# Kernel tuning notes

Measured on AMD Instinct MI355X. Metric: run time of the kernel, lower is better.

The kernel has to match this reference:

```python
import jax, jax.numpy as jnp
import numpy as np
from jax import lax

B, T, D, H, S = 256, 512, 256, 512, 8


def setup_inputs() -> dict:
    key = jax.random.key(0)
    ks = jax.random.split(key, 8)
    bound = 1.0 / np.sqrt(H)  # torch LSTMCell/Linear default init scale
    u = lambda k_, shp: jax.random.uniform(k_, shp, jnp.float32, -bound, bound)
    _input = jax.random.normal(ks[0], (B, T, D), jnp.float32)
    h0 = jax.random.normal(ks[1], (B, H), jnp.float32)
    c0 = jax.random.normal(ks[2], (B, H), jnp.float32)
    W_ih = u(ks[3], (4 * H, D))
    W_hh = u(ks[4], (4 * H, H))
    b_ih = u(ks[5], (4 * H,))
    b_hh = u(ks[6], (4 * H,))
    W_lin = u(ks[7], (D, H))
    b_lin = jnp.zeros((D,), jnp.float32)
    # random skip weights per module logic: w1~Bern; w2=1 if w1==0 else Bern; first S steps (1,0)
    rng = np.random.default_rng(0)
    w1 = rng.integers(0, 2, T)
    w2 = np.where(w1 == 0, 1, rng.integers(0, 2, T))
    w1[:S] = 1
    w2[:S] = 0
    return {
        "_input": _input, "h0": h0, "c0": c0,
        "W_ih": W_ih, "W_hh": W_hh, "b_ih": b_ih, "b_hh": b_hh,
        "W_lin": W_lin, "b_lin": b_lin,
        "w1": jnp.asarray(w1, jnp.int32), "w2": jnp.asarray(w2, jnp.int32),
        "time_steps": T, "skip_size": S,
    }


def _lstm_cell(x, h, c, W_ih, W_hh, b_ih, b_hh):
    gates = x @ W_ih.T + b_ih + h @ W_hh.T + b_hh  # [B, 4H]
    i, f, g, o = jnp.split(gates, 4, axis=-1)
    i, f, o = jax.nn.sigmoid(i), jax.nn.sigmoid(f), jax.nn.sigmoid(o)
    c_new = f * c + i * jnp.tanh(g)
    h_new = o * jnp.tanh(c_new)
    return h_new, c_new


def reference(_input, h0, c0, W_ih, W_hh, b_ih, b_hh, W_lin, b_lin, w1, w2, time_steps, skip_size):
    # decoder-mode RSCN: feed previous linear(h) as next input
    buf_h = jnp.repeat(h0[None], skip_size, axis=0)  # FIFO queue as ring buffer [S,B,H]
    buf_c = jnp.repeat(c0[None], skip_size, axis=0)

    def step(carry, xs):
        h_feed, h, c, bh, bc = carry
        w1t, w2t, t = xs
        h_new, c_new = _lstm_cell(h_feed, h, c, W_ih, W_hh, b_ih, b_hh)
        pos = t % skip_size
        skip_h, skip_c = bh[pos], bc[pos]  # queue.get() (oldest)
        bh = bh.at[pos].set(h_new)          # queue.put(new)
        bc = bc.at[pos].set(c_new)
        a = w1t.astype(h_new.dtype)
        b = w2t.astype(h_new.dtype)
        norm = 1.0 / (a + b)
        comb_h = (a * h_new + b * jnp.tanh(skip_h)) * norm
        comb_c = (a * c_new + b * jnp.tanh(skip_c)) * norm
        out = comb_h @ W_lin.T + b_lin  # [B, D]
        return (out, comb_h, comb_c, bh, bc), out

    xs = (w1[:time_steps], w2[:time_steps], jnp.arange(time_steps))
    carry0 = (_input[:, 0, :], h0, c0, buf_h, buf_c)
    (_, h_fin, c_fin, _, _), outs = lax.scan(step, carry0, xs)
    return outs.transpose(1, 0, 2), h_fin, c_fin  # [B,T,D], final (h, c)
```

## Files before the change

kernel.cpp:

```cpp
#include <hip/hip_runtime.h>
#include <math.h>

#define BB 256
#define TT 512
#define DD 256
#define HH 512
#define SS 8
#define G4H 2048
#define BH (BB*HH)
#define OUT_BASE ((size_t)BB*TT*DD)
#define NGRP 16
#define GR 16
#define XSLOT_U32 4096

typedef _Float16 f16;
typedef __attribute__((ext_vector_type(8))) _Float16 f16x8;
typedef __attribute__((ext_vector_type(4))) float    f32x4;

__device__ __forceinline__ float sigm(float x) { return 1.f / (1.f + __expf(-x)); }
__device__ __forceinline__ float ftanh(float x) {
  x = fminf(15.f, fmaxf(-15.f, x));
  float e = __expf(-2.f * x);
  return (1.f - e) / (1.f + e);
}


__global__ __launch_bounds__(256) void prep_wbig16(
    const float* __restrict__ W_ih, const float* __restrict__ W_hh,
    const float* __restrict__ W_lin, f16* __restrict__ Wbig16)
{
  __shared__ float As[64][20];
  __shared__ float Bs[16][68];
  const int n0 = blockIdx.x * 64;
  const int j0 = blockIdx.y * 64;
  const int tid = threadIdx.x;
  const int tn = tid >> 4, tj = tid & 15;
  float acc[4][4] = {};
  for (int k0 = 0; k0 < DD; k0 += 16) {
    { int r = tid >> 2, c = (tid & 3) * 4;
      *(float4*)&As[r][c] = *(const float4*)&W_ih[(size_t)(n0 + r) * DD + k0 + c]; }
    { int r = tid >> 4, c = (tid & 15) * 4;
      *(float4*)&Bs[r][c] = *(const float4*)&W_lin[(size_t)(k0 + r) * HH + j0 + c]; }
    __syncthreads();
    #pragma unroll
    for (int k = 0; k < 16; ++k) {
      float a[4], bv[4];
      #pragma unroll
      for (int i = 0; i < 4; ++i) a[i] = As[tn*4+i][k];
      #pragma unroll
      for (int m = 0; m < 4; ++m) bv[m] = Bs[k][tj*4+m];
      #pragma unroll
      for (int i = 0; i < 4; ++i)
        #pragma unroll
        for (int m = 0; m < 4; ++m)
          acc[i][m] = fmaf(a[i], bv[m], acc[i][m]);
    }
    __syncthreads();
  }
  #pragma unroll
  for (int i = 0; i < 4; ++i) {
    int n = n0 + tn*4 + i;
    #pragma unroll
    for (int m = 0; m < 4; ++m) {
      int j = j0 + tj*4 + m;
      Wbig16[(size_t)n*HH + j] = (f16)(acc[i][m] + W_hh[(size_t)n*HH + j]);
    }
  }
}

__global__ void prep_bias(const float* __restrict__ b_ih, const float* __restrict__ b_hh,
                          const float* __restrict__ W_ih, const float* __restrict__ b_lin,
                          float* __restrict__ bias0, float* __restrict__ bias1)
{
  int n = blockIdx.x * 256 + threadIdx.x;
  float s = b_ih[n] + b_hh[n];
  float d = 0.f;
  for (int k = 0; k < DD; ++k) d = fmaf(W_ih[(size_t)n*DD + k], b_lin[k], d);
  bias0[n] = s;
  bias1[n] = s + d;
}

#define NIH (G4H*DD)
#define NHH (G4H*HH)
__global__ void prep_cvtw(const float* __restrict__ W_ih, const float* __restrict__ W_hh,
                          const float* __restrict__ W_lin,
                          f16* __restrict__ Wih16, f16* __restrict__ Whh16,
                          f16* __restrict__ Wlin16)
{
  int e = blockIdx.x * 256 + threadIdx.x;
  if (e < NIH) Wih16[e] = (f16)W_ih[e];
  else if (e < NIH + NHH) Whh16[e - NIH] = (f16)W_hh[e - NIH];
  else Wlin16[e - NIH - NHH] = (f16)W_lin[e - NIH - NHH];
}

__global__ void prep_init(const float* __restrict__ x0, const float* __restrict__ h0,
                          const float* __restrict__ c0,
                          const int* __restrict__ w1, const int* __restrict__ w2,
                          float* __restrict__ bh, float* __restrict__ bc,
                          f16* __restrict__ x0hi, f16* __restrict__ x0lo,
                          f16* __restrict__ h0hi, f16* __restrict__ h0lo,
                          float4* __restrict__ stepc,
                          int* __restrict__ flags)
{
  int e = blockIdx.x * 256 + threadIdx.x;
  int r = e & (BH - 1);
  bh[e] = h0[r];
  bc[e] = c0[r];
  if (e < BH) {
    float v = h0[e];
    f16 hi = (f16)v;
    h0hi[e] = hi;
    h0lo[e] = (f16)(v - (float)hi);
  }
  if (e < BB*DD) {
    int b = e >> 8, d = e & 255;
    float v = x0[(size_t)b*(TT*DD) + d];
    f16 hi = (f16)v;
    x0hi[e] = hi;
    x0lo[e] = (f16)(v - (float)hi);
  }
  if (e < TT) {
    float a1 = (float)w1[e], a2 = (float)w2[e];
    stepc[e] = make_float4(a1, a2, 1.f / (a1 + a2), 0.f);
  }
  if (e < 256) flags[e] = 0;
}


__device__ __forceinline__ void stageG(const unsigned* __restrict__ Xs,
                                       f16* lds, int tid) {
  const int lane = tid & 63;
  const int wv = tid >> 6;
  #pragma unroll
  for (int i = 0; i < 2; ++i) {
    int r = wv * 2 + i;
    const char* src = (const char*)Xs + (size_t)r * 1024 +
                      (size_t)((lane ^ r) & 63) * 16;
    __builtin_amdgcn_global_load_lds(
        (const __attribute__((address_space(1))) void*)src,
        (__attribute__((address_space(3))) void*)((char*)lds + r * 1024),
        16, 0, 0x11 );
  }
}

__device__ __forceinline__ void gemm16(const f16x8 (&wA)[16], const f16x8 (&wB)[16],
                                       const f16* lds, int lane,
                                       f32x4& acc0, f32x4& acc1) {
  const int r  = lane & 15;
  const int kc = lane >> 4;
  const int rb = r * 1024;
  #pragma unroll
  for (int ks = 0; ks < 16; ++ks) {
    int u = ks * 4 + kc;
    f16x8 a = *(const f16x8*)((const char*)lds + rb + ((u ^ r) << 4));
    acc0 = __builtin_amdgcn_mfma_f32_16x16x32_f16(a, wA[ks], acc0, 0, 0, 0);
    acc1 = __builtin_amdgcn_mfma_f32_16x16x32_f16(a, wB[ks], acc1, 0, 0, 0);
  }
}

__global__ __launch_bounds__(512, 2) void lstm_persist(
    const f16* __restrict__ x0hi, const f16* __restrict__ x0lo,
    const f16* __restrict__ h0hi, const f16* __restrict__ h0lo,
    const float* __restrict__ c0,
    const f16* __restrict__ Wih16, const f16* __restrict__ Whh16,
    const f16* __restrict__ Wbig16, const f16* __restrict__ Wlin16,
    const float* __restrict__ bias0, const float* __restrict__ bias1,
    const float* __restrict__ b_lin,
    const float4* __restrict__ stepc,
    unsigned* __restrict__ X,
    float* __restrict__ bh, float* __restrict__ bc,
    int* __restrict__ flags,
    float* __restrict__ outp)
{
  __shared__ f16 LdsA[8192];
  __shared__ float gbuf[4096];

  const int tid  = threadIdx.x;
  const int lane = tid & 63;
  const int wv   = tid >> 6;
  const int bid  = blockIdx.x;
  const bool isG = bid < 128;
  const int grp  = isG ? (bid & 15) : (bid - 128);
  const int role = bid >> 4;
  const int b0   = grp * GR;
  const int r16  = lane & 15;
  const int kc   = lane >> 4;
  const int ksel = kc * 8;

  int* gflag = flags + grp * 16;

  int rowA, rowB;
  const f16* wsrc;
  if (isG) {
    rowA = (wv & 3) * 512 + role * 64 + (wv >> 2) * 32 + r16;
    rowB = rowA + 16;
    wsrc = Wbig16;
  } else {
    rowA = wv * 32 + r16;
    rowB = rowA + 16;
    wsrc = Wlin16;
  }
  f16x8 wA[16], wB[16];
  #pragma unroll
  for (int ks = 0; ks < 16; ++ks) {
    wA[ks] = *(const f16x8*)(wsrc + (size_t)rowA * HH + ks * 32 + ksel);
    wB[ks] = *(const f16x8*)(wsrc + (size_t)rowB * HH + ks * 32 + ksel);
  }

  if (isG) {
    int   eidx[2];
    float creg[2];
    const int jl = tid & 63;
    const int jg = role * 64 + jl;
    const float bI = bias1[jg],        bF = bias1[512 + jg];
    const float bG = bias1[1024 + jg], bO = bias1[1536 + jg];
    #pragma unroll
    for (int i = 0; i < 2; ++i) {
      int c = i * 512 + tid;
      int bl = c >> 6;
      eidx[i] = (b0 + bl) * HH + jg;
      creg[i] = c0[eidx[i]];
    }

    for (int t = 0; t < TT; ++t) {
      if (t > 0) {
        if (tid < 8) {
          while (__hip_atomic_load(&gflag[tid], __ATOMIC_RELAXED,
                                   __HIP_MEMORY_SCOPE_AGENT) < t) {}
        } else if (tid == 8 && t >= 4) {
          while (__hip_atomic_load(&gflag[8], __ATOMIC_RELAXED,
                                   __HIP_MEMORY_SCOPE_AGENT) < t - 3) {}
        }
        __syncthreads();
        stageG(X + (size_t)(((t - 1) & 3) * NGRP + grp) * XSLOT_U32, LdsA, tid);
      }

      const float4 sc = stepc[t];
      const int pos = t & (SS - 1);
      float shv[2], scv[2];
      #pragma unroll
      for (int i = 0; i < 2; ++i) {
        int bx = pos * BH + eidx[i];
        shv[i] = bh[bx];
        scv[i] = bc[bx];
      }

      f32x4 acc0, acc1;
      #pragma unroll
      for (int i = 0; i < 4; ++i) { acc0[i] = 0.f; acc1[i] = 0.f; }
      if (t == 0) {
        const f16* arh = x0hi + (size_t)(b0 + r16) * DD;
        const f16* arl = x0lo + (size_t)(b0 + r16) * DD;
        const f16* wap = Wih16 + (size_t)rowA * DD;
        const f16* wbp = Wih16 + (size_t)rowB * DD;
        #pragma unroll
        for (int ks = 0; ks < 8; ++ks) {
          int ko = ks * 32 + ksel;
          f16x8 wa = *(const f16x8*)(wap + ko);
          f16x8 wb = *(const f16x8*)(wbp + ko);
          f16x8 ah = *(const f16x8*)(arh + ko);
          f16x8 al = *(const f16x8*)(arl + ko);
          acc0 = __builtin_amdgcn_mfma_f32_16x16x32_f16(ah, wa, acc0, 0, 0, 0);
          acc1 = __builtin_amdgcn_mfma_f32_16x16x32_f16(ah, wb, acc1, 0, 0, 0);
          acc0 = __builtin_amdgcn_mfma_f32_16x16x32_f16(al, wa, acc0, 0, 0, 0);
          acc1 = __builtin_amdgcn_mfma_f32_16x16x32_f16(al, wb, acc1, 0, 0, 0);
        }
        const f16* brh = h0hi + (size_t)(b0 + r16) * HH;
        const f16* brl = h0lo + (size_t)(b0 + r16) * HH;
        const f16* qap = Whh16 + (size_t)rowA * HH;
        const f16* qbp = Whh16 + (size_t)rowB * HH;
        #pragma unroll
        for (int ks = 0; ks < 16; ++ks) {
          int ko = ks * 32 + ksel;
          f16x8 wa = *(const f16x8*)(qap + ko);
          f16x8 wb = *(const f16x8*)(qbp + ko);
          f16x8 ah = *(const f16x8*)(brh + ko);
          f16x8 al = *(const f16x8*)(brl + ko);
          acc0 = __builtin_amdgcn_mfma_f32_16x16x32_f16(ah, wa, acc0, 0, 0, 0);
          acc1 = __builtin_amdgcn_mfma_f32_16x16x32_f16(ah, wb, acc1, 0, 0, 0);
          acc0 = __builtin_amdgcn_mfma_f32_16x16x32_f16(al, wa, acc0, 0, 0, 0);
          acc1 = __builtin_amdgcn_mfma_f32_16x16x32_f16(al, wb, acc1, 0, 0, 0);
        }
      } else {
        __syncthreads();
        gemm16(wA, wB, LdsA, lane, acc0, acc1);
      }

      {
        const int g4 = wv & 3, jh = wv >> 2;
        #pragma unroll
        for (int rg = 0; rg < 4; ++rg) {
          int m  = kc * 4 + rg;
          int j0 = jh * 32 + r16;
          int cs0 = (j0      + 16 * kc) & 63;
          int cs1 = (j0 + 16 + 16 * kc) & 63;
          gbuf[g4 * 1024 + m * 64 + cs0] = acc0[rg];
          gbuf[g4 * 1024 + m * 64 + cs1] = acc1[rg];
        }
      }
      __syncthreads();

      const float a1 = sc.x, a2 = sc.y, nrm = sc.z;
      float baI = bI, baF = bF, baG = bG, baO = bO;
      if (t == 0) {
        baI = bias0[jg];        baF = bias0[512 + jg];
        baG = bias0[1024 + jg]; baO = bias0[1536 + jg];
      }
      unsigned* Xw = X + (size_t)((t & 3) * NGRP + grp) * XSLOT_U32;
      float hnv[2], cnv[2], chv[2];
      #pragma unroll
      for (int i = 0; i < 2; ++i) {
        int c = i * 512 + tid;
        int bl = c >> 6;
        int jj = c & 63;
        int gofs = bl * 64 + ((jj + 16 * (bl >> 2)) & 63);
        float pi = gbuf[gofs]        + baI;
        float pf = gbuf[1024 + gofs] + baF;
        float pg = gbuf[2048 + gofs] + baG;
        float po = gbuf[3072 + gofs] + baO;
        float i_ = sigm(pi), f_ = sigm(pf), o_ = sigm(po), g_ = ftanh(pg);
        float cnew = fmaf(f_, creg[i], i_ * g_);
        float hnew = o_ * ftanh(cnew);
        float ch = (a1 * hnew + a2 * ftanh(shv[i])) * nrm;
        hnv[i] = hnew; cnv[i] = cnew; chv[i] = ch;
        f16 hv = (f16)ch;
        unsigned hb = (unsigned)*(const unsigned short*)&hv;
        unsigned part = (unsigned)__shfl_xor((int)hb, 1);
        if ((tid & 1) == 0)
          __hip_atomic_store(&Xw[bl * 256 + (jg >> 1)], hb | (part << 16),
                             __ATOMIC_RELAXED, __HIP_MEMORY_SCOPE_AGENT);
      }
      __syncthreads();
      if (tid == 0)
        __hip_atomic_store(&gflag[role], t + 1, __ATOMIC_RELAXED,
                           __HIP_MEMORY_SCOPE_AGENT);

      #pragma unroll
      for (int i = 0; i < 2; ++i) {
        float cc = (a1 * cnv[i] + a2 * ftanh(scv[i])) * nrm;
        creg[i] = cc;
        int bx = pos * BH + eidx[i];
        bh[bx] = hnv[i];
        bc[bx] = cnv[i];
        if (t == TT - 1) {
          __builtin_nontemporal_store(chv[i], &outp[OUT_BASE + eidx[i]]);
          __builtin_nontemporal_store(cc,     &outp[OUT_BASE + BH + eidx[i]]);
        }
      }
    }
  } else {
    const float bld0 = b_lin[rowA];
    const float bld1 = b_lin[rowB];
    for (int s = 0; s < TT; ++s) {
      if (tid < 8) {
        while (__hip_atomic_load(&gflag[tid], __ATOMIC_RELAXED,
                                 __HIP_MEMORY_SCOPE_AGENT) < s + 1) {}
      }
      __syncthreads();
      stageG(X + (size_t)((s & 3) * NGRP + grp) * XSLOT_U32, LdsA, tid);
      __syncthreads();
      f32x4 acc0, acc1;
      #pragma unroll
      for (int i = 0; i < 4; ++i) { acc0[i] = 0.f; acc1[i] = 0.f; }
      gemm16(wA, wB, LdsA, lane, acc0, acc1);
      __syncthreads();
      if (tid == 0)
        __hip_atomic_store(&gflag[8], s + 1, __ATOMIC_RELAXED,
                           __HIP_MEMORY_SCOPE_AGENT);
      const size_t tbase = (size_t)s * DD + wv * 32 + r16;
      #pragma unroll
      for (int rg = 0; rg < 4; ++rg) {
        int m = kc * 4 + rg;
        __builtin_nontemporal_store(acc0[rg] + bld0,
                                    &outp[(size_t)(b0 + m) * (TT*DD) + tbase]);
        __builtin_nontemporal_store(acc1[rg] + bld1,
                                    &outp[(size_t)(b0 + m) * (TT*DD) + tbase + 16]);
      }
    }
  }
}


extern "C" void kernel_launch(void* const* d_in, const int* in_sizes, int n_in,
                              void* d_out, int out_size, void* d_ws, size_t ws_size,
                              hipStream_t stream)
{
  const float* x0    = (const float*)d_in[0];
  const float* h0    = (const float*)d_in[1];
  const float* c0    = (const float*)d_in[2];
  const float* W_ih  = (const float*)d_in[3];
  const float* W_hh  = (const float*)d_in[4];
  const float* b_ih  = (const float*)d_in[5];
  const float* b_hh  = (const float*)d_in[6];
  const float* W_lin = (const float*)d_in[7];
  const float* b_lin = (const float*)d_in[8];
  const int*   w1    = (const int*)d_in[9];
  const int*   w2    = (const int*)d_in[10];

  char* p = (char*)d_ws;
  f16* Wbig16 = (f16*)p;            p += (size_t)G4H*HH*2;
  f16* Wih16  = (f16*)p;            p += (size_t)G4H*DD*2;
  f16* Whh16  = (f16*)p;            p += (size_t)G4H*HH*2;
  f16* Wlin16 = (f16*)p;            p += (size_t)DD*HH*2;
  f16* x0hi   = (f16*)p;            p += (size_t)BB*DD*2;
  f16* x0lo   = (f16*)p;            p += (size_t)BB*DD*2;
  f16* h0hi   = (f16*)p;            p += (size_t)BH*2;
  f16* h0lo   = (f16*)p;            p += (size_t)BH*2;
  unsigned* X = (unsigned*)p;       p += (size_t)4*NGRP*XSLOT_U32*4;
  float* bh   = (float*)p;          p += (size_t)SS*BH*4;
  float* bc   = (float*)p;          p += (size_t)SS*BH*4;
  float* bias0= (float*)p;          p += G4H*4;
  float* bias1= (float*)p;          p += G4H*4;
  float4* stepc = (float4*)p;       p += (size_t)TT*16;
  int*  flags = (int*)p;            p += 256*4;
  float* outp = (float*)d_out;

  hipLaunchKernelGGL(prep_wbig16, dim3(32, 8), dim3(256), 0, stream,
                     W_ih, W_hh, W_lin, Wbig16);
  hipLaunchKernelGGL(prep_bias, dim3(8), dim3(256), 0, stream,
                     b_ih, b_hh, W_ih, b_lin, bias0, bias1);
  hipLaunchKernelGGL(prep_cvtw, dim3(6656), dim3(256), 0, stream,
                     W_ih, W_hh, W_lin, Wih16, Whh16, Wlin16);
  hipLaunchKernelGGL(prep_init, dim3(4096), dim3(256), 0, stream,
                     x0, h0, c0, w1, w2, bh, bc, x0hi, x0lo, h0hi, h0lo, stepc, flags);

  hipLaunchKernelGGL(lstm_persist, dim3(128 + NGRP), dim3(512), 0, stream,
                     x0hi, x0lo, h0hi, h0lo, c0, Wih16, Whh16, Wbig16, Wlin16,
                     bias0, bias1, b_lin, stepc, X, bh, bc, flags, outp);
}
```

Baseline: 1.660 ms.

## Publish skip-only hidden state early when w1 is zero and widen X ring to 8

When a step's w1 weight is zero (after the first S steps), the combined hidden state depends only on tanh of the skip buffer entry. So gate blocks now compute and publish it before doing their own GEMM, and signal the step flag early. This lets the next step and the output-projection blocks proceed without waiting for the current step's gate computation. The X ring buffer grows from 4 to 8 slots so producers can run further ahead. Synchronisation gets more intricate, and the extra slots add workspace memory.

New measurement: 1.686 ms. About the same (+1.5%).

```diff
diff --git a/kernel.cpp b/kernel.cpp
--- a/kernel.cpp
+++ b/kernel.cpp
@@ -11,6 +11,7 @@
 #define OUT_BASE ((size_t)BB*TT*DD)
 #define NGRP 16
 #define GR 16
+#define XRING 8
 #define XSLOT_U32 4096
 
 typedef _Float16 f16;
@@ -223,26 +224,52 @@
     }
 
     for (int t = 0; t < TT; ++t) {
+      const float4 sc = stepc[t];
+      const int pos = t & (SS - 1);
+      float shv[2], scv[2];
+      #pragma unroll
+      for (int i = 0; i < 2; ++i) {
+        int bx = pos * BH + eidx[i];
+        shv[i] = bh[bx];
+        scv[i] = bc[bx];
+      }
+
+      const bool early = (t >= SS) && (sc.x == 0.0f);
+      unsigned* Xw = X + (size_t)((t & (XRING-1)) * NGRP + grp) * XSLOT_U32;
+
+      if (early) {
+        if (tid == 0) {
+          while (__hip_atomic_load(&gflag[8], __ATOMIC_RELAXED,
+                                   __HIP_MEMORY_SCOPE_AGENT) < t - 7) {}
+        }
+        __syncthreads();
+        #pragma unroll
+        for (int i = 0; i < 2; ++i) {
+          int c = i * 512 + tid;
+          int bl = c >> 6;
+          f16 hv = (f16)ftanh(shv[i]);
+          unsigned hb = (unsigned)*(const unsigned short*)&hv;
+          unsigned part = (unsigned)__shfl_xor((int)hb, 1);
+          if ((tid & 1) == 0)
+            __hip_atomic_store(&Xw[bl * 256 + (jg >> 1)], hb | (part << 16),
+                               __ATOMIC_RELAXED, __HIP_MEMORY_SCOPE_AGENT);
+        }
+        __syncthreads();
+        if (tid == 0)
+          __hip_atomic_store(&gflag[role], t + 1, __ATOMIC_RELAXED,
+                             __HIP_MEMORY_SCOPE_AGENT);
+      }
+
       if (t > 0) {
         if (tid < 8) {
           while (__hip_atomic_load(&gflag[tid], __ATOMIC_RELAXED,
                                    __HIP_MEMORY_SCOPE_AGENT) < t) {}
-        } else if (tid == 8 && t >= 4) {
+        } else if (tid == 8 && t >= XRING) {
           while (__hip_atomic_load(&gflag[8], __ATOMIC_RELAXED,
-                                   __HIP_MEMORY_SCOPE_AGENT) < t - 3) {}
+                                   __HIP_MEMORY_SCOPE_AGENT) < t - (XRING-1)) {}
         }
         __syncthreads();
-        stageG(X + (size_t)(((t - 1) & 3) * NGRP + grp) * XSLOT_U32, LdsA, tid);
-      }
-
-      const float4 sc = stepc[t];
-      const int pos = t & (SS - 1);
-      float shv[2], scv[2];
-      #pragma unroll
-      for (int i = 0; i < 2; ++i) {
-        int bx = pos * BH + eidx[i];
-        shv[i] = bh[bx];
-        scv[i] = bc[bx];
+        stageG(X + (size_t)(((t - 1) & (XRING-1)) * NGRP + grp) * XSLOT_U32, LdsA, tid);
       }
 
       f32x4 acc0, acc1;
@@ -306,7 +333,6 @@
         baI = bias0[jg];        baF = bias0[512 + jg];
         baG = bias0[1024 + jg]; baO = bias0[1536 + jg];
       }
-      unsigned* Xw = X + (size_t)((t & 3) * NGRP + grp) * XSLOT_U32;
       float hnv[2], cnv[2], chv[2];
       #pragma unroll
       for (int i = 0; i < 2; ++i) {
@@ -323,15 +349,17 @@
         float hnew = o_ * ftanh(cnew);
         float ch = (a1 * hnew + a2 * ftanh(shv[i])) * nrm;
         hnv[i] = hnew; cnv[i] = cnew; chv[i] = ch;
-        f16 hv = (f16)ch;
-        unsigned hb = (unsigned)*(const unsigned short*)&hv;
-        unsigned part = (unsigned)__shfl_xor((int)hb, 1);
-        if ((tid & 1) == 0)
-          __hip_atomic_store(&Xw[bl * 256 + (jg >> 1)], hb | (part << 16),
-                             __ATOMIC_RELAXED, __HIP_MEMORY_SCOPE_AGENT);
+        if (!early) {
+          f16 hv = (f16)ch;
+          unsigned hb = (unsigned)*(const unsigned short*)&hv;
+          unsigned part = (unsigned)__shfl_xor((int)hb, 1);
+          if ((tid & 1) == 0)
+            __hip_atomic_store(&Xw[bl * 256 + (jg >> 1)], hb | (part << 16),
+                               __ATOMIC_RELAXED, __HIP_MEMORY_SCOPE_AGENT);
+        }
       }
       __syncthreads();
-      if (tid == 0)
+      if (!early && tid == 0)
         __hip_atomic_store(&gflag[role], t + 1, __ATOMIC_RELAXED,
                            __HIP_MEMORY_SCOPE_AGENT);
 
@@ -357,7 +385,7 @@
                                  __HIP_MEMORY_SCOPE_AGENT) < s + 1) {}
       }
       __syncthreads();
-      stageG(X + (size_t)((s & 3) * NGRP + grp) * XSLOT_U32, LdsA, tid);
+      stageG(X + (size_t)((s & (XRING-1)) * NGRP + grp) * XSLOT_U32, LdsA, tid);
       __syncthreads();
       f32x4 acc0, acc1;
       #pragma unroll
@@ -406,7 +434,7 @@
   f16* x0lo   = (f16*)p;            p += (size_t)BB*DD*2;
   f16* h0hi   = (f16*)p;            p += (size_t)BH*2;
   f16* h0lo   = (f16*)p;            p += (size_t)BH*2;
-  unsigned* X = (unsigned*)p;       p += (size_t)4*NGRP*XSLOT_U32*4;
+  unsigned* X = (unsigned*)p;       p += (size_t)XRING*NGRP*XSLOT_U32*4;
   float* bh   = (float*)p;          p += (size_t)SS*BH*4;
   float* bc   = (float*)p;          p += (size_t)SS*BH*4;
   float* bias0= (float*)p;          p += G4H*4;
```

## Use per-wave counter flags and stripe-wise X staging with deeper ring

Applied to the files above, without the earlier changes.

Replaces block-level flag signalling with per-wave atomic fetch-add counters, so each wave waits only on the producer role whose stripe of h it needs and stages that stripe itself. The X layout changes so that each role's 64 columns form a contiguous 2KB stripe, with a matching swizzle in the gemm reader. The X ring grows from 4 to 8 slots to loosen back-pressure from the linear-output blocks. This removes several __syncthreads and single-thread polls from the recurrent critical path, but it relies on s_waitcnt plus relaxed atomics for visibility and adds more atomic traffic.

Result: slower. 3.507 ms (+111.2%).

```diff
diff --git a/kernel.cpp b/kernel.cpp
--- a/kernel.cpp
+++ b/kernel.cpp
@@ -11,6 +11,7 @@
 #define OUT_BASE ((size_t)BB*TT*DD)
 #define NGRP 16
 #define GR 16
+#define XRING 8
 #define XSLOT_U32 4096
 
 typedef _Float16 f16;
@@ -127,18 +128,17 @@
 }
 
 
-__device__ __forceinline__ void stageG(const unsigned* __restrict__ Xs,
-                                       f16* lds, int tid) {
-  const int lane = tid & 63;
-  const int wv = tid >> 6;
+__device__ __forceinline__ void stage_stripe(const unsigned* __restrict__ Xs,
+                                             int w, f16* lds, int lane) {
   #pragma unroll
   for (int i = 0; i < 2; ++i) {
-    int r = wv * 2 + i;
-    const char* src = (const char*)Xs + (size_t)r * 1024 +
-                      (size_t)((lane ^ r) & 63) * 16;
+    int q = i * 64 + lane;
+    int row = q >> 3, u = q & 7;
+    const char* src = (const char*)Xs + w * 2048 + row * 128 +
+                      (((u ^ (row & 7))) << 4);
     __builtin_amdgcn_global_load_lds(
         (const __attribute__((address_space(1))) void*)src,
-        (__attribute__((address_space(3))) void*)((char*)lds + r * 1024),
+        (__attribute__((address_space(3))) void*)((char*)lds + w * 2048 + i * 1024),
         16, 0, 0x11 );
   }
 }
@@ -148,11 +148,13 @@
                                        f32x4& acc0, f32x4& acc1) {
   const int r  = lane & 15;
   const int kc = lane >> 4;
-  const int rb = r * 1024;
   #pragma unroll
   for (int ks = 0; ks < 16; ++ks) {
-    int u = ks * 4 + kc;
-    f16x8 a = *(const f16x8*)((const char*)lds + rb + ((u ^ r) << 4));
+    int k0 = ks * 32 + kc * 8;
+    int role = k0 >> 6;
+    int u = (k0 & 63) >> 3;
+    int off = role * 2048 + r * 128 + ((u ^ (r & 7)) << 4);
+    f16x8 a = *(const f16x8*)((const char*)lds + off);
     acc0 = __builtin_amdgcn_mfma_f32_16x16x32_f16(a, wA[ks], acc0, 0, 0, 0);
     acc1 = __builtin_amdgcn_mfma_f32_16x16x32_f16(a, wB[ks], acc1, 0, 0, 0);
   }
@@ -223,18 +225,6 @@
     }
 
     for (int t = 0; t < TT; ++t) {
-      if (t > 0) {
-        if (tid < 8) {
-          while (__hip_atomic_load(&gflag[tid], __ATOMIC_RELAXED,
-                                   __HIP_MEMORY_SCOPE_AGENT) < t) {}
-        } else if (tid == 8 && t >= 4) {
-          while (__hip_atomic_load(&gflag[8], __ATOMIC_RELAXED,
-                                   __HIP_MEMORY_SCOPE_AGENT) < t - 3) {}
-        }
-        __syncthreads();
-        stageG(X + (size_t)(((t - 1) & 3) * NGRP + grp) * XSLOT_U32, LdsA, tid);
-      }
-
       const float4 sc = stepc[t];
       const int pos = t & (SS - 1);
       float shv[2], scv[2];
@@ -244,6 +234,19 @@
         shv[i] = bh[bx];
         scv[i] = bc[bx];
       }
+
+      if (t > 0) {
+        const int target = 8 * t;
+        while (__hip_atomic_load(&gflag[wv], __ATOMIC_RELAXED,
+                                 __HIP_MEMORY_SCOPE_AGENT) < target) {}
+        if (wv == 0 && t >= XRING) {
+          while (__hip_atomic_load(&gflag[8], __ATOMIC_RELAXED,
+                                   __HIP_MEMORY_SCOPE_AGENT) < 8 * (t - (XRING-1))) {}
+        }
+        stage_stripe(X + (size_t)(((t - 1) & (XRING-1)) * NGRP + grp) * XSLOT_U32,
+                     wv, LdsA, lane);
+      }
+      __syncthreads();
 
       f32x4 acc0, acc1;
       #pragma unroll
@@ -282,7 +285,6 @@
           acc1 = __builtin_amdgcn_mfma_f32_16x16x32_f16(al, wb, acc1, 0, 0, 0);
         }
       } else {
-        __syncthreads();
         gemm16(wA, wB, LdsA, lane, acc0, acc1);
       }
 
@@ -306,7 +308,7 @@
         baI = bias0[jg];        baF = bias0[512 + jg];
         baG = bias0[1024 + jg]; baO = bias0[1536 + jg];
       }
-      unsigned* Xw = X + (size_t)((t & 3) * NGRP + grp) * XSLOT_U32;
+      unsigned* Xw = X + (size_t)((t & (XRING-1)) * NGRP + grp) * XSLOT_U32;
       float hnv[2], cnv[2], chv[2];
       #pragma unroll
       for (int i = 0; i < 2; ++i) {
@@ -327,13 +329,13 @@
         unsigned hb = (unsigned)*(const unsigned short*)&hv;
         unsigned part = (unsigned)__shfl_xor((int)hb, 1);
         if ((tid & 1) == 0)
-          __hip_atomic_store(&Xw[bl * 256 + (jg >> 1)], hb | (part << 16),
+          __hip_atomic_store(&Xw[role * 512 + bl * 32 + (jl >> 1)], hb | (part << 16),
                              __ATOMIC_RELAXED, __HIP_MEMORY_SCOPE_AGENT);
       }
-      __syncthreads();
-      if (tid == 0)
-        __hip_atomic_store(&gflag[role], t + 1, __ATOMIC_RELAXED,
-                           __HIP_MEMORY_SCOPE_AGENT);
+      asm volatile("s_waitcnt vmcnt(0)" ::: "memory");
+      if (lane == 0)
+        __hip_atomic_fetch_add(&gflag[role], 1, __ATOMIC_RELAXED,
+                               __HIP_MEMORY_SCOPE_AGENT);
 
       #pragma unroll
       for (int i = 0; i < 2; ++i) {
@@ -352,21 +354,19 @@
     const float bld0 = b_lin[rowA];
     const float bld1 = b_lin[rowB];
     for (int s = 0; s < TT; ++s) {
-      if (tid < 8) {
-        while (__hip_atomic_load(&gflag[tid], __ATOMIC_RELAXED,
-                                 __HIP_MEMORY_SCOPE_AGENT) < s + 1) {}
-      }
+      const int target = 8 * (s + 1);
+      while (__hip_atomic_load(&gflag[wv], __ATOMIC_RELAXED,
+                               __HIP_MEMORY_SCOPE_AGENT) < target) {}
+      stage_stripe(X + (size_t)((s & (XRING-1)) * NGRP + grp) * XSLOT_U32,
+                   wv, LdsA, lane);
       __syncthreads();
-      stageG(X + (size_t)((s & 3) * NGRP + grp) * XSLOT_U32, LdsA, tid);
-      __syncthreads();
+      if (tid == 0)
+        __hip_atomic_store(&gflag[8], 8 * (s + 1), __ATOMIC_RELAXED,
+                           __HIP_MEMORY_SCOPE_AGENT);
       f32x4 acc0, acc1;
       #pragma unroll
       for (int i = 0; i < 4; ++i) { acc0[i] = 0.f; acc1[i] = 0.f; }
       gemm16(wA, wB, LdsA, lane, acc0, acc1);
-      __syncthreads();
-      if (tid == 0)
-        __hip_atomic_store(&gflag[8], s + 1, __ATOMIC_RELAXED,
-                           __HIP_MEMORY_SCOPE_AGENT);
       const size_t tbase = (size_t)s * DD + wv * 32 + r16;
       #pragma unroll
       for (int rg = 0; rg < 4; ++rg) {
@@ -376,6 +376,7 @@
         __builtin_nontemporal_store(acc1[rg] + bld1,
                                     &outp[(size_t)(b0 + m) * (TT*DD) + tbase + 16]);
       }
+      __syncthreads();
     }
   }
 }
@@ -406,7 +407,7 @@
   f16* x0lo   = (f16*)p;            p += (size_t)BB*DD*2;
   f16* h0hi   = (f16*)p;            p += (size_t)BH*2;
   f16* h0lo   = (f16*)p;            p += (size_t)BH*2;
-  unsigned* X = (unsigned*)p;       p += (size_t)4*NGRP*XSLOT_U32*4;
+  unsigned* X = (unsigned*)p;       p += (size_t)XRING*NGRP*XSLOT_U32*4;
   float* bh   = (float*)p;          p += (size_t)SS*BH*4;
   float* bc   = (float*)p;          p += (size_t)SS*BH*4;
   float* bias0= (float*)p;          p += G4H*4;
```
